# Kernel tuning notes

Measured on AMD Instinct MI355X. Metric: run time of the kernel, lower is better.

## Reference

```python
import jax, jax.numpy as jnp
import numpy as np
from jax import lax

K = 3          # kernel_size
STRIDE = 1
PAD = 1        # (K-1)//2
C = 64         # channels
GC = 16        # group_channels
G = C // GC    # groups = 4
NS = 1         # new_size = ratio * stride
EPS = 1e-5


def mish(x):
    return x * jnp.tanh(jax.nn.softplus(x))


def setup_inputs() -> dict:
    key = jax.random.key(0)
    ks = jax.random.split(key, 4)
    B, H, W = 2, 256, 256
    c1_in = C * K * 2 + G * K * K      # 420
    c1_out = C * NS * NS // 4          # 16
    return {
        "inputs": jax.random.normal(ks[0], (B, C, H, W), jnp.float32),
        "conv1_w": jax.random.normal(ks[1], (c1_out, c1_in, 1, 1), jnp.float32) * 0.05,
        "conv1_b": jnp.zeros((c1_out,), jnp.float32),
        "conv2_w": jax.random.normal(ks[2], (C // 4, C // 4, 3, 3), jnp.float32) * 0.05,
        "conv2_b": jnp.zeros((C // 4,), jnp.float32),
        "conv3_w": jax.random.normal(ks[3], (G * K * K, C // 4, 1, 1), jnp.float32) * 0.05,
        "conv3_b": jnp.zeros((G * K * K,), jnp.float32),
        "bn_gamma": jnp.ones((c1_out,), jnp.float32),
        "bn_beta": jnp.zeros((c1_out,), jnp.float32),
        "bn_mean": jnp.zeros((c1_out,), jnp.float32),
        "bn_var": jnp.ones((c1_out,), jnp.float32),
    }


def _unfold(x, h, w):
    # torch.nn.Unfold(K, 1, PAD, STRIDE): output channel layout (C, kh, kw)
    xp = jnp.pad(x, ((0, 0), (0, 0), (PAD, PAD), (PAD, PAD)))
    cols = [xp[:, :, ki:ki + (h - 1) * STRIDE + 1:STRIDE,
                     kj:kj + (w - 1) * STRIDE + 1:STRIDE]
            for ki in range(K) for kj in range(K)]
    return jnp.stack(cols, axis=2)  # (b, C, K*K, h, w)


def reference(inputs, conv1_w, conv1_b, conv2_w, conv2_b, conv3_w, conv3_b,
              bn_gamma, bn_beta, bn_mean, bn_var):
    b, _, Wd, Hd = inputs.shape
    h = (Wd + 2 * PAD - K) // STRIDE + 1
    w = (Hd + 2 * PAD - K) // STRIDE + 1
    x = _unfold(inputs, h, w).reshape(b, G, GC, K, K, h, w)
    # multi-axis max pooling over (group_channels, kh, kw)
    m_gc = x.max(axis=2).reshape(b, -1, h, w)  # (b, G*K*K, h, w)
    m_kh = x.max(axis=3).reshape(b, -1, h, w)  # (b, C*K, h, w)
    m_kw = x.max(axis=4).reshape(b, -1, h, w)  # (b, C*K, h, w)
    weight = jnp.concatenate([m_gc, m_kh, m_kw], axis=1)  # (b, 420, h, w)
    # conv1 (1x1) + Mish
    weight = mish(jnp.einsum('bihw,oi->bohw', weight, conv1_w[:, :, 0, 0])
                  + conv1_b[None, :, None, None])                  # (b, 16, h, w)
    c = C // 4
    # rearrange 'b (c n1 n2) h w -> (b h w) c n1 n2'
    wn = weight.reshape(b, c, NS, NS, h, w).transpose(0, 4, 5, 1, 2, 3)
    wn = wn.reshape(b * h * w, c, NS, NS)
    wn = lax.conv_general_dilated(wn, conv2_w, (1, 1), ((1, 1), (1, 1)),
                                  dimension_numbers=('NCHW', 'OIHW', 'NCHW'))
    wn = wn + conv2_b[None, :, None, None]
    # rearrange back '(b h w) c n1 n2 -> b (c n1 n2) h w'
    wn = wn.reshape(b, h, w, c, NS, NS).transpose(0, 3, 4, 5, 1, 2)
    wn = wn.reshape(b, c * NS * NS, h, w)
    # BatchNorm (inference form with running stats)
    scale = bn_gamma / jnp.sqrt(bn_var + EPS)
    wn = wn * scale[None, :, None, None] + (bn_beta - bn_mean * scale)[None, :, None, None]
    weight = weight * mish(wn)
    # conv3 (1x1) -> per-pixel attention logits
    weight = jnp.einsum('bihw,oi->bohw', weight, conv3_w[:, :, 0, 0]) \
             + conv3_b[None, :, None, None]                          # (b, G*K*K, h, w)
    weight = jax.nn.softmax(weight.reshape(b, G, 1, K * K, NS * NS, h, w), axis=3)
    # softmax-weighted patch aggregation
    agg = jnp.sum(x.reshape(b, G, GC, K * K, 1, h, w) * weight, axis=3)  # (b,G,GC,NS^2,h,w)
    # fold with kernel=stride=NS (non-overlapping): pure reshape/transpose
    out = agg.reshape(b, C, NS, NS, h, w).transpose(0, 1, 4, 2, 5, 3)
    return out.reshape(b, C, h * NS, w * NS)
```

## Files before the change

kernel.cpp:

```cpp
#include <hip/hip_runtime.h>
#include <hip/hip_bf16.h>
#include <math.h>

#define Cch 64
#define Hh  256
#define Ww  256
#define HW  (Hh * Ww)

#define WS_WC2  8192
#define WS_SC   8448
#define WS_OFF  8464

#define SROW 67
#define SCH  201
#define SGRP 3216
#define LDSY 12864
#define LDS_TOT (12864 + 5120)

typedef __attribute__((ext_vector_type(8))) short bf16x8;
typedef __attribute__((ext_vector_type(4))) float f32x4;

__device__ __forceinline__ float mishf(float x) {
    float e  = __expf(fminf(x, 15.0f));
    float n  = 1.0f + e;
    float n2 = n * n;
    float t  = __fdividef(n2 - 1.0f, n2 + 1.0f);
    return x > 15.0f ? x : x * t;
}

__device__ __forceinline__ unsigned packbf(float a, float b) {
    unsigned short ua = __builtin_bit_cast(unsigned short, __float2bfloat16(a));
    unsigned short ub = __builtin_bit_cast(unsigned short, __float2bfloat16(b));
    return (unsigned)ua | ((unsigned)ub << 16);
}

__device__ __forceinline__ float conv1_wval(const float* w1, int g, int m,
                                            int cc, int j) {
    int c = g * 16 + cc;
    if (j < 3)  return w1[m * 420 + 36 + c * 3 + j];
    if (j < 6)  return w1[m * 420 + 228 + c * 3 + (j - 3)];
    if (j == 6) return (cc < 9) ? w1[m * 420 + g * 9 + cc] : 0.0f;
    return 0.0f;
}

__global__ __launch_bounds__(256) void prep_kernel(
    const float* __restrict__ w1, const float* __restrict__ w2,
    const float* __restrict__ b2,
    const float* __restrict__ gamma, const float* __restrict__ beta,
    const float* __restrict__ mean,  const float* __restrict__ var,
    float* __restrict__ ws)
{
    unsigned* wsu = (unsigned*)ws;
    const int tid = threadIdx.x;

    for (int idx = tid; idx < 1024; idx += 256) {
        int g = idx >> 8, s = (idx >> 6) & 3, lane = idx & 63;
        int m = lane & 15, half = lane >> 4;
        int cc = 4 * s + half;
        unsigned hi[4], lo[4];
        #pragma unroll
        for (int jp = 0; jp < 4; ++jp) {
            float hv[2], lv[2];
            #pragma unroll
            for (int e = 0; e < 2; ++e) {
                float v  = conv1_wval(w1, g, m, cc, jp * 2 + e);
                float hf = __bfloat162float(__float2bfloat16(v));
                hv[e] = hf;
                lv[e] = v - hf;
            }
            hi[jp] = packbf(hv[0], hv[1]);
            lo[jp] = packbf(lv[0], lv[1]);
        }
        int b0 = idx * 8;
        #pragma unroll
        for (int i = 0; i < 4; ++i) { wsu[b0 + i] = hi[i]; wsu[b0 + 4 + i] = lo[i]; }
    }

    for (int idx = tid; idx < 256; idx += 256) {
        int o = idx / 16, i = idx % 16;
        ws[WS_WC2 + idx] = w2[o * 144 + i * 9 + 4];
    }
    if (tid < 16) {
        float sc = gamma[tid] * rsqrtf(var[tid] + 1e-5f);
        ws[WS_SC + tid]  = sc;
        ws[WS_OFF + tid] = b2[tid] * sc + beta[tid] - mean[tid] * sc;
    }
}

__global__ __launch_bounds__(256) void revo_kernel(
    const float* __restrict__ in,
    const float* __restrict__ b1,
    const float* __restrict__ w3, const float* __restrict__ b3,
    const float* __restrict__ ws,
    float* __restrict__ out)
{
    const int tid  = threadIdx.x;
    const int g    = __builtin_amdgcn_readfirstlane(tid >> 6);
    const int l    = tid & 63;

    const int bid     = blockIdx.x;
    const int logical = ((bid & 7) << 8) + (bid >> 3);
    const int wseg = logical & 3;
    const int h    = (logical >> 2) & (Hh - 1);
    const int b    = logical >> 10;
    const int wbase = wseg * 64;
    const int w     = wbase + l;

    __shared__ float lds[LDS_TOT];
    float* stageg = lds + g * SGRP;
    float* ldsy   = lds + LDSY;

    const float* base = in + ((size_t)b * Cch + g * 16) * HW;

    {
        #pragma unroll 6
        for (int it = 0; it < 48; ++it) {
            int c = it / 3, r = it % 3;
            int hr = h + r - 1;
            float v = 0.0f, vh = 0.0f;
            if (hr >= 0 && hr < Hh) {
                const float* rowp = base + (size_t)c * HW + (size_t)hr * Ww;
                v = rowp[wbase + l];
                if (l == 0 && wseg > 0)  vh = rowp[wbase - 1];
                if (l == 63 && wseg < 3) vh = rowp[wbase + 64];
            }
            stageg[c * SCH + r * SROW + 1 + l] = v;
            if (l == 0)  stageg[c * SCH + r * SROW]      = vh;
            if (l == 63) stageg[c * SCH + r * SROW + 65] = vh;
        }
    }

    const int ln = l & 15, half = l >> 4;
    f32x4 acc[4];
    #pragma unroll
    for (int t = 0; t < 4; ++t) acc[t] = (f32x4){0.f, 0.f, 0.f, 0.f};

    {
        const uint4* wa = (const uint4*)ws;
        uint4 Ahi[4], Alo[4];
        #pragma unroll
        for (int s = 0; s < 4; ++s) {
            int ix = ((g * 4 + s) * 64 + l) * 2;
            Ahi[s] = wa[ix];
            Alo[s] = wa[ix + 1];
        }

        #pragma unroll
        for (int s = 0; s < 4; ++s) {
            const int cc = 4 * s + half;
            const float* chp = stageg + cc * SCH;
            const bool hasgc = (cc < 9);
            const int rp = cc / 3, dp = cc % 3;

            #pragma unroll
            for (int t = 0; t < 4; ++t) {
                const int p = 16 * t + ln;
                float a0 = chp[p],           a1 = chp[p + 1],       a2 = chp[p + 2];
                float b0 = chp[SROW + p],    b1v = chp[SROW + p + 1], b2v = chp[SROW + p + 2];
                float c0 = chp[2*SROW + p],  c1 = chp[2*SROW + p + 1], c2 = chp[2*SROW + p + 2];

                float mkh0 = fmaxf(fmaxf(a0, b0), c0);
                float mkh1 = fmaxf(fmaxf(a1, b1v), c1);
                float mkh2 = fmaxf(fmaxf(a2, b2v), c2);
                float mkw0 = fmaxf(fmaxf(a0, a1), a2);
                float mkw1 = fmaxf(fmaxf(b0, b1v), b2v);
                float mkw2 = fmaxf(fmaxf(c0, c1), c2);

                float gv = 0.0f;
                if (hasgc) {
                    const float* gp2 = stageg + rp * SROW + dp + p;
                    gv = gp2[0];
                    #pragma unroll
                    for (int c2i = 1; c2i < 16; ++c2i)
                        gv = fmaxf(gv, gp2[c2i * SCH]);
                }

                uint4 bv;
                bv.x = packbf(mkh0, mkh1);
                bv.y = packbf(mkh2, mkw0);
                bv.z = packbf(mkw1, mkw2);
                bv.w = packbf(gv, 0.0f);

                acc[t] = __builtin_amdgcn_mfma_f32_16x16x32_bf16(
                    __builtin_bit_cast(bf16x8, Ahi[s]),
                    __builtin_bit_cast(bf16x8, bv), acc[t], 0, 0, 0);
                acc[t] = __builtin_amdgcn_mfma_f32_16x16x32_bf16(
                    __builtin_bit_cast(bf16x8, Alo[s]),
                    __builtin_bit_cast(bf16x8, bv), acc[t], 0, 0, 0);
            }
        }
    }

    #pragma unroll
    for (int t = 0; t < 4; ++t)
        *(f32x4*)&ldsy[(g * 64 + 16 * t + ln) * 20 + 4 * half] = acc[t];
    __syncthreads();

    float feat[16];
    {
        #pragma unroll
        for (int r4 = 0; r4 < 4; ++r4) {
            f32x4 rr = (f32x4){0.f, 0.f, 0.f, 0.f};
            #pragma unroll
            for (int gp = 0; gp < 4; ++gp)
                rr += *(const f32x4*)&ldsy[(gp * 64 + l) * 20 + 4 * r4];
            #pragma unroll
            for (int j = 0; j < 4; ++j)
                feat[4 * r4 + j] = rr[j];
        }
        #pragma unroll
        for (int o = 0; o < 16; ++o) feat[o] = mishf(feat[o] + b1[o]);
    }

    float feat2[16];
    {
        const float* wc2 = ws + WS_WC2;
        const float* sc  = ws + WS_SC;
        const float* off = ws + WS_OFF;
        #pragma unroll
        for (int o = 0; o < 16; ++o) {
            float acc2 = 0.0f;
            #pragma unroll
            for (int i = 0; i < 16; ++i)
                acc2 = fmaf(wc2[o * 16 + i], feat[i], acc2);
            feat2[o] = feat[o] * mishf(acc2 * sc[o] + off[o]);
        }
    }

    float att[9];
    {
        float mx = -1e30f;
        #pragma unroll
        for (int k = 0; k < 9; ++k) {
            float acc2 = b3[g * 9 + k];
            const float* r = w3 + (g * 9 + k) * 16;
            #pragma unroll
            for (int i = 0; i < 16; ++i)
                acc2 = fmaf(r[i], feat2[i], acc2);
            att[k] = acc2;
            mx = fmaxf(mx, acc2);
        }
        float s = 0.0f;
        #pragma unroll
        for (int k = 0; k < 9; ++k) { att[k] = __expf(att[k] - mx); s += att[k]; }
        float inv = __fdividef(1.0f, s);
        #pragma unroll
        for (int k = 0; k < 9; ++k) att[k] *= inv;
    }

    float* ob = out + (((size_t)b * Cch + g * 16) * Hh + h) * Ww + w;
    #pragma unroll 4
    for (int c = 0; c < 16; ++c) {
        const float* chp = stageg + c * SCH;
        float a0 = chp[l],          a1 = chp[l + 1],          a2 = chp[l + 2];
        float b0 = chp[SROW + l],   b1v = chp[SROW + l + 1],  b2v = chp[SROW + l + 2];
        float c0 = chp[2*SROW + l], c1 = chp[2*SROW + l + 1], c2 = chp[2*SROW + l + 2];
        float acc2 = 0.0f;
        acc2 = fmaf(a0,  att[0], acc2);
        acc2 = fmaf(a1,  att[1], acc2);
        acc2 = fmaf(a2,  att[2], acc2);
        acc2 = fmaf(b0,  att[3], acc2);
        acc2 = fmaf(b1v, att[4], acc2);
        acc2 = fmaf(b2v, att[5], acc2);
        acc2 = fmaf(c0,  att[6], acc2);
        acc2 = fmaf(c1,  att[7], acc2);
        acc2 = fmaf(c2,  att[8], acc2);
        ob[(size_t)c * HW] = acc2;
    }
}

extern "C" void kernel_launch(void* const* d_in, const int* in_sizes, int n_in,
                              void* d_out, int out_size, void* d_ws, size_t ws_size,
                              hipStream_t stream) {
    const float* in    = (const float*)d_in[0];
    const float* w1    = (const float*)d_in[1];
    const float* b1    = (const float*)d_in[2];
    const float* w2    = (const float*)d_in[3];
    const float* b2    = (const float*)d_in[4];
    const float* w3    = (const float*)d_in[5];
    const float* b3    = (const float*)d_in[6];
    const float* gamma = (const float*)d_in[7];
    const float* beta  = (const float*)d_in[8];
    const float* mean  = (const float*)d_in[9];
    const float* var   = (const float*)d_in[10];
    float* out = (float*)d_out;
    float* ws  = (float*)d_ws;

    hipLaunchKernelGGL(prep_kernel, dim3(1), dim3(256), 0, stream,
                       w1, w2, b2, gamma, beta, mean, var, ws);

    hipLaunchKernelGGL(revo_kernel, dim3(2048), dim3(256), 0, stream,
                       in, b1, w3, b3, ws, out);
}
```

Measured before the change: 112.6 us.

## Replace LDS input staging with direct register loads and double-buffered chunks

Drops the shared-memory staging of the 3x16x66 input window. Each thread now loads its own 3x3 neighbourhood per channel straight from global memory into registers, in double-buffered 4-channel chunks, with boundary masking done in registers. The group-channel max is computed in registers and fed as a fifth MFMA k-slice with a repacked weight layout. Inputs are reloaded from global (cache) for the aggregation phase instead of reread from LDS. This cuts LDS footprint to raise occupancy (launch bounds 256,4), at the cost of 9x redundant global/cache loads per pixel and higher register pressure.

```diff
diff --git a/kernel.cpp b/kernel.cpp
--- a/kernel.cpp
+++ b/kernel.cpp
@@ -5,17 +5,11 @@
 #define Cch 64
 #define Hh  256
 #define Ww  256
-#define HW  (Hh * Ww)
-
-#define WS_WC2  8192
-#define WS_SC   8448
-#define WS_OFF  8464
-
-#define SROW 67
-#define SCH  201
-#define SGRP 3216
-#define LDSY 12864
-#define LDS_TOT (12864 + 5120)
+#define HW  (Hh * 256)
+
+#define WS_WC2  10240
+#define WS_SC   10496
+#define WS_OFF  10512
 
 typedef __attribute__((ext_vector_type(8))) short bf16x8;
 typedef __attribute__((ext_vector_type(4))) float f32x4;
@@ -35,12 +29,15 @@
 }
 
 __device__ __forceinline__ float conv1_wval(const float* w1, int g, int m,
-                                            int cc, int j) {
-    int c = g * 16 + cc;
-    if (j < 3)  return w1[m * 420 + 36 + c * 3 + j];
-    if (j < 6)  return w1[m * 420 + 228 + c * 3 + (j - 3)];
-    if (j == 6) return (cc < 9) ? w1[m * 420 + g * 9 + cc] : 0.0f;
-    return 0.0f;
+                                            int s, int qt, int j) {
+    if (s < 4) {
+        if (j >= 6) return 0.0f;
+        int c = g * 16 + 4 * s + qt;
+        return (j < 3) ? w1[m * 420 + 36 + c * 3 + j]
+                       : w1[m * 420 + 228 + c * 3 + (j - 3)];
+    }
+    int k = 8 * qt + j;
+    return (k < 9) ? w1[m * 420 + g * 9 + k] : 0.0f;
 }
 
 __global__ __launch_bounds__(256) void prep_kernel(
@@ -53,17 +50,16 @@
     unsigned* wsu = (unsigned*)ws;
     const int tid = threadIdx.x;
 
-    for (int idx = tid; idx < 1024; idx += 256) {
-        int g = idx >> 8, s = (idx >> 6) & 3, lane = idx & 63;
-        int m = lane & 15, half = lane >> 4;
-        int cc = 4 * s + half;
+    for (int idx = tid; idx < 1280; idx += 256) {
+        int g = idx / 320, s = (idx / 64) % 5, lane = idx % 64;
+        int m = lane & 15, qt = lane >> 4;
         unsigned hi[4], lo[4];
         #pragma unroll
         for (int jp = 0; jp < 4; ++jp) {
             float hv[2], lv[2];
             #pragma unroll
             for (int e = 0; e < 2; ++e) {
-                float v  = conv1_wval(w1, g, m, cc, jp * 2 + e);
+                float v  = conv1_wval(w1, g, m, s, qt, jp * 2 + e);
                 float hf = __bfloat162float(__float2bfloat16(v));
                 hv[e] = hf;
                 lv[e] = v - hf;
@@ -87,7 +83,99 @@
     }
 }
 
-__global__ __launch_bounds__(256) void revo_kernel(
+#define LDS_FENCE() do {                                             \
+    asm volatile("s_waitcnt lgkmcnt(0)" ::: "memory");               \
+    __builtin_amdgcn_sched_barrier(0);                               \
+} while (0)
+#define ORDER_FENCE() do {                                           \
+    asm volatile("" ::: "memory");                                   \
+    __builtin_amdgcn_sched_barrier(0);                               \
+} while (0)
+
+#define LOAD9(dst, cb) do {                                          \
+    const float* r0_ = (cb) + (size_t)hmc * Ww + w;                  \
+    const float* r1_ = (cb) + (size_t)h   * Ww + w;                  \
+    const float* r2_ = (cb) + (size_t)hpc * Ww + w;                  \
+    (dst)[0] = r0_[offm]; (dst)[1] = r0_[0]; (dst)[2] = r0_[offp];   \
+    (dst)[3] = r1_[offm]; (dst)[4] = r1_[0]; (dst)[5] = r1_[offp];   \
+    (dst)[6] = r2_[offm]; (dst)[7] = r2_[0]; (dst)[8] = r2_[offp];   \
+} while (0)
+
+#define CHUNK_LOAD(P, S) do {                                        \
+    _Pragma("unroll")                                                \
+    for (int i_ = 0; i_ < 4; ++i_)                                   \
+        LOAD9(&(P)[9 * i_], base + (size_t)(4 * (S) + i_) * HW);     \
+} while (0)
+
+#define PHA_PROC(P, S, INIT) do {                                    \
+    const uint4* wa_ = (const uint4*)ws;                             \
+    uint4 Ahi_ = wa_[((g * 5 + (S)) * 64 + l) * 2];                  \
+    uint4 Alo_ = wa_[((g * 5 + (S)) * 64 + l) * 2 + 1];              \
+    _Pragma("unroll")                                                \
+    for (int i_ = 0; i_ < 4; ++i_) {                                 \
+        float* q_ = &(P)[9 * i_];                                    \
+        q_[0] = (okhm && okm) ? q_[0] : 0.0f;                        \
+        q_[1] =  okhm         ? q_[1] : 0.0f;                        \
+        q_[2] = (okhm && okp) ? q_[2] : 0.0f;                        \
+        q_[3] =  okm          ? q_[3] : 0.0f;                        \
+        q_[5] =  okp          ? q_[5] : 0.0f;                        \
+        q_[6] = (okhp && okm) ? q_[6] : 0.0f;                        \
+        q_[7] =  okhp         ? q_[7] : 0.0f;                        \
+        q_[8] = (okhp && okp) ? q_[8] : 0.0f;                        \
+        if ((INIT) && i_ == 0) {                                     \
+            _Pragma("unroll")                                        \
+            for (int k_ = 0; k_ < 9; ++k_) gmax[k_] = q_[k_];        \
+        } else {                                                     \
+            _Pragma("unroll")                                        \
+            for (int k_ = 0; k_ < 9; ++k_)                           \
+                gmax[k_] = fmaxf(gmax[k_], q_[k_]);                  \
+        }                                                            \
+        float mkh0 = fmaxf(fmaxf(q_[0], q_[3]), q_[6]);              \
+        float mkh1 = fmaxf(fmaxf(q_[1], q_[4]), q_[7]);              \
+        float mkh2 = fmaxf(fmaxf(q_[2], q_[5]), q_[8]);              \
+        float mkw0 = fmaxf(fmaxf(q_[0], q_[1]), q_[2]);              \
+        float mkw1 = fmaxf(fmaxf(q_[3], q_[4]), q_[5]);              \
+        float mkw2 = fmaxf(fmaxf(q_[6], q_[7]), q_[8]);              \
+        uint4 v_;                                                    \
+        v_.x = packbf(mkh0, mkh1);                                   \
+        v_.y = packbf(mkh2, mkw0);                                   \
+        v_.z = packbf(mkw1, mkw2);                                   \
+        v_.w = 0u;                                                   \
+        slab[g][l * 5 + i_] = v_;                                    \
+    }                                                                \
+    LDS_FENCE();                                                     \
+    _Pragma("unroll")                                                \
+    for (int t_ = 0; t_ < 4; ++t_) {                                 \
+        uint4 bv_ = slab[g][(16 * t_ + ln) * 5 + half];              \
+        acc[t_] = __builtin_amdgcn_mfma_f32_16x16x32_bf16(           \
+            __builtin_bit_cast(bf16x8, Ahi_),                        \
+            __builtin_bit_cast(bf16x8, bv_), acc[t_], 0, 0, 0);      \
+        acc[t_] = __builtin_amdgcn_mfma_f32_16x16x32_bf16(           \
+            __builtin_bit_cast(bf16x8, Alo_),                        \
+            __builtin_bit_cast(bf16x8, bv_), acc[t_], 0, 0, 0);      \
+    }                                                                \
+    ORDER_FENCE();                                                   \
+} while (0)
+
+#define AGG_PROC(P, S) do {                                          \
+    _Pragma("unroll")                                                \
+    for (int i_ = 0; i_ < 4; ++i_) {                                 \
+        const float* q_ = &(P)[9 * i_];                              \
+        float a2_ = 0.0f;                                            \
+        a2_ = fmaf((okhm && okm) ? q_[0] : 0.0f, att[0], a2_);       \
+        a2_ = fmaf( okhm         ? q_[1] : 0.0f, att[1], a2_);       \
+        a2_ = fmaf((okhm && okp) ? q_[2] : 0.0f, att[2], a2_);       \
+        a2_ = fmaf( okm          ? q_[3] : 0.0f, att[3], a2_);       \
+        a2_ = fmaf( q_[4],                       att[4], a2_);       \
+        a2_ = fmaf( okp          ? q_[5] : 0.0f, att[5], a2_);       \
+        a2_ = fmaf((okhp && okm) ? q_[6] : 0.0f, att[6], a2_);       \
+        a2_ = fmaf( okhp         ? q_[7] : 0.0f, att[7], a2_);       \
+        a2_ = fmaf((okhp && okp) ? q_[8] : 0.0f, att[8], a2_);       \
+        ob[(size_t)(4 * (S) + i_) * HW] = a2_;                       \
+    }                                                                \
+} while (0)
+
+__global__ __launch_bounds__(256, 4) void revo_kernel(
     const float* __restrict__ in,
     const float* __restrict__ b1,
     const float* __restrict__ w3, const float* __restrict__ b3,
@@ -103,113 +191,79 @@
     const int wseg = logical & 3;
     const int h    = (logical >> 2) & (Hh - 1);
     const int b    = logical >> 10;
-    const int wbase = wseg * 64;
-    const int w     = wbase + l;
-
-    __shared__ float lds[LDS_TOT];
-    float* stageg = lds + g * SGRP;
-    float* ldsy   = lds + LDSY;
+    const int w    = wseg * 64 + l;
+
+    __shared__ uint4 slab[4][320];
+    __shared__ float ldsy[4][64][17];
 
     const float* base = in + ((size_t)b * Cch + g * 16) * HW;
 
-    {
-        #pragma unroll 6
-        for (int it = 0; it < 48; ++it) {
-            int c = it / 3, r = it % 3;
-            int hr = h + r - 1;
-            float v = 0.0f, vh = 0.0f;
-            if (hr >= 0 && hr < Hh) {
-                const float* rowp = base + (size_t)c * HW + (size_t)hr * Ww;
-                v = rowp[wbase + l];
-                if (l == 0 && wseg > 0)  vh = rowp[wbase - 1];
-                if (l == 63 && wseg < 3) vh = rowp[wbase + 64];
-            }
-            stageg[c * SCH + r * SROW + 1 + l] = v;
-            if (l == 0)  stageg[c * SCH + r * SROW]      = vh;
-            if (l == 63) stageg[c * SCH + r * SROW + 65] = vh;
-        }
-    }
+    const bool okm = (w > 0);
+    const bool okp = (w < Ww - 1);
+    const int offm = okm ? -1 : 0;
+    const int offp = okp ?  1 : 0;
+
+    const int hm = h - 1, hp = h + 1;
+    const bool okhm = (hm >= 0), okhp = (hp < Hh);
+    const int hmc = okhm ? hm : 0;
+    const int hpc = okhp ? hp : Hh - 1;
 
     const int ln = l & 15, half = l >> 4;
+
     f32x4 acc[4];
     #pragma unroll
     for (int t = 0; t < 4; ++t) acc[t] = (f32x4){0.f, 0.f, 0.f, 0.f};
 
+    float gmax[9];
+    float pA[36], pB[36];
+
+    CHUNK_LOAD(pA, 0);
+    CHUNK_LOAD(pB, 1);
+    PHA_PROC(pA, 0, 1);
+    CHUNK_LOAD(pA, 2);
+    PHA_PROC(pB, 1, 0);
+    CHUNK_LOAD(pB, 3);
+    PHA_PROC(pA, 2, 0);
+    PHA_PROC(pB, 3, 0);
+
     {
         const uint4* wa = (const uint4*)ws;
-        uint4 Ahi[4], Alo[4];
-        #pragma unroll
-        for (int s = 0; s < 4; ++s) {
-            int ix = ((g * 4 + s) * 64 + l) * 2;
-            Ahi[s] = wa[ix];
-            Alo[s] = wa[ix + 1];
+        uint4 Ahi4 = wa[((g * 5 + 4) * 64 + l) * 2];
+        uint4 Alo4 = wa[((g * 5 + 4) * 64 + l) * 2 + 1];
+        uint4 v0; v0.x = packbf(gmax[0], gmax[1]); v0.y = packbf(gmax[2], gmax[3]);
+                  v0.z = packbf(gmax[4], gmax[5]); v0.w = packbf(gmax[6], gmax[7]);
+        uint4 v1; v1.x = packbf(gmax[8], 0.0f); v1.y = 0u; v1.z = 0u; v1.w = 0u;
+        uint4 vz; vz.x = 0u; vz.y = 0u; vz.z = 0u; vz.w = 0u;
+        slab[g][l * 5 + 0] = v0;
+        slab[g][l * 5 + 1] = v1;
+        slab[g][l * 5 + 2] = vz;
+        slab[g][l * 5 + 3] = vz;
+        LDS_FENCE();
+        #pragma unroll
+        for (int t = 0; t < 4; ++t) {
+            uint4 bv = slab[g][(16 * t + ln) * 5 + half];
+            acc[t] = __builtin_amdgcn_mfma_f32_16x16x32_bf16(
+                __builtin_bit_cast(bf16x8, Ahi4),
+                __builtin_bit_cast(bf16x8, bv), acc[t], 0, 0, 0);
+            acc[t] = __builtin_amdgcn_mfma_f32_16x16x32_bf16(
+                __builtin_bit_cast(bf16x8, Alo4),
+                __builtin_bit_cast(bf16x8, bv), acc[t], 0, 0, 0);
         }
-
-        #pragma unroll
-        for (int s = 0; s < 4; ++s) {
-            const int cc = 4 * s + half;
-            const float* chp = stageg + cc * SCH;
-            const bool hasgc = (cc < 9);
-            const int rp = cc / 3, dp = cc % 3;
-
-            #pragma unroll
-            for (int t = 0; t < 4; ++t) {
-                const int p = 16 * t + ln;
-                float a0 = chp[p],           a1 = chp[p + 1],       a2 = chp[p + 2];
-                float b0 = chp[SROW + p],    b1v = chp[SROW + p + 1], b2v = chp[SROW + p + 2];
-                float c0 = chp[2*SROW + p],  c1 = chp[2*SROW + p + 1], c2 = chp[2*SROW + p + 2];
-
-                float mkh0 = fmaxf(fmaxf(a0, b0), c0);
-                float mkh1 = fmaxf(fmaxf(a1, b1v), c1);
-                float mkh2 = fmaxf(fmaxf(a2, b2v), c2);
-                float mkw0 = fmaxf(fmaxf(a0, a1), a2);
-                float mkw1 = fmaxf(fmaxf(b0, b1v), b2v);
-                float mkw2 = fmaxf(fmaxf(c0, c1), c2);
-
-                float gv = 0.0f;
-                if (hasgc) {
-                    const float* gp2 = stageg + rp * SROW + dp + p;
-                    gv = gp2[0];
-                    #pragma unroll
-                    for (int c2i = 1; c2i < 16; ++c2i)
-                        gv = fmaxf(gv, gp2[c2i * SCH]);
-                }
-
-                uint4 bv;
-                bv.x = packbf(mkh0, mkh1);
-                bv.y = packbf(mkh2, mkw0);
-                bv.z = packbf(mkw1, mkw2);
-                bv.w = packbf(gv, 0.0f);
-
-                acc[t] = __builtin_amdgcn_mfma_f32_16x16x32_bf16(
-                    __builtin_bit_cast(bf16x8, Ahi[s]),
-                    __builtin_bit_cast(bf16x8, bv), acc[t], 0, 0, 0);
-                acc[t] = __builtin_amdgcn_mfma_f32_16x16x32_bf16(
-                    __builtin_bit_cast(bf16x8, Alo[s]),
-                    __builtin_bit_cast(bf16x8, bv), acc[t], 0, 0, 0);
-            }
-        }
+        ORDER_FENCE();
     }
 
     #pragma unroll
     for (int t = 0; t < 4; ++t)
-        *(f32x4*)&ldsy[(g * 64 + 16 * t + ln) * 20 + 4 * half] = acc[t];
+        #pragma unroll
+        for (int j = 0; j < 4; ++j)
+            ldsy[g][16 * t + ln][4 * half + j] = acc[t][j];
     __syncthreads();
 
     float feat[16];
-    {
-        #pragma unroll
-        for (int r4 = 0; r4 < 4; ++r4) {
-            f32x4 rr = (f32x4){0.f, 0.f, 0.f, 0.f};
-            #pragma unroll
-            for (int gp = 0; gp < 4; ++gp)
-                rr += *(const f32x4*)&ldsy[(gp * 64 + l) * 20 + 4 * r4];
-            #pragma unroll
-            for (int j = 0; j < 4; ++j)
-                feat[4 * r4 + j] = rr[j];
-        }
-        #pragma unroll
-        for (int o = 0; o < 16; ++o) feat[o] = mishf(feat[o] + b1[o]);
+    #pragma unroll
+    for (int o = 0; o < 16; ++o) {
+        float t = ldsy[0][l][o] + ldsy[1][l][o] + ldsy[2][l][o] + ldsy[3][l][o];
+        feat[o] = mishf(t + b1[o]);
     }
 
     float feat2[16];
@@ -219,11 +273,11 @@
         const float* off = ws + WS_OFF;
         #pragma unroll
         for (int o = 0; o < 16; ++o) {
-            float acc2 = 0.0f;
+            float a2 = 0.0f;
             #pragma unroll
             for (int i = 0; i < 16; ++i)
-                acc2 = fmaf(wc2[o * 16 + i], feat[i], acc2);
-            feat2[o] = feat[o] * mishf(acc2 * sc[o] + off[o]);
+                a2 = fmaf(wc2[o * 16 + i], feat[i], a2);
+            feat2[o] = feat[o] * mishf(a2 * sc[o] + off[o]);
         }
     }
 
@@ -232,13 +286,13 @@
         float mx = -1e30f;
         #pragma unroll
         for (int k = 0; k < 9; ++k) {
-            float acc2 = b3[g * 9 + k];
+            float a2 = b3[g * 9 + k];
             const float* r = w3 + (g * 9 + k) * 16;
             #pragma unroll
             for (int i = 0; i < 16; ++i)
-                acc2 = fmaf(r[i], feat2[i], acc2);
-            att[k] = acc2;
-            mx = fmaxf(mx, acc2);
+                a2 = fmaf(r[i], feat2[i], a2);
+            att[k] = a2;
+            mx = fmaxf(mx, a2);
         }
         float s = 0.0f;
         #pragma unroll
@@ -249,24 +303,14 @@
     }
 
     float* ob = out + (((size_t)b * Cch + g * 16) * Hh + h) * Ww + w;
-    #pragma unroll 4
-    for (int c = 0; c < 16; ++c) {
-        const float* chp = stageg + c * SCH;
-        float a0 = chp[l],          a1 = chp[l + 1],          a2 = chp[l + 2];
-        float b0 = chp[SROW + l],   b1v = chp[SROW + l + 1],  b2v = chp[SROW + l + 2];
-        float c0 = chp[2*SROW + l], c1 = chp[2*SROW + l + 1], c2 = chp[2*SROW + l + 2];
-        float acc2 = 0.0f;
-        acc2 = fmaf(a0,  att[0], acc2);
-        acc2 = fmaf(a1,  att[1], acc2);
-        acc2 = fmaf(a2,  att[2], acc2);
-        acc2 = fmaf(b0,  att[3], acc2);
-        acc2 = fmaf(b1v, att[4], acc2);
-        acc2 = fmaf(b2v, att[5], acc2);
-        acc2 = fmaf(c0,  att[6], acc2);
-        acc2 = fmaf(c1,  att[7], acc2);
-        acc2 = fmaf(c2,  att[8], acc2);
-        ob[(size_t)c * HW] = acc2;
-    }
+    CHUNK_LOAD(pA, 0);
+    CHUNK_LOAD(pB, 1);
+    AGG_PROC(pA, 0);
+    CHUNK_LOAD(pA, 2);
+    AGG_PROC(pB, 1);
+    CHUNK_LOAD(pB, 3);
+    AGG_PROC(pA, 2);
+    AGG_PROC(pB, 3);
 }
 
 extern "C" void kernel_launch(void* const* d_in, const int* in_sizes, int n_in,
```

Result: slower. 282.8 us (+151.1%).

## Replace LDS staging with direct register loads and per-wave pixel tiling

Applied to the files above, without the earlier changes.

Stops staging the 3x3 neighbourhood of each group's 16 channels in LDS. Each wave now takes 16 pixels, and its four lane quarters cover the four channel groups. Each lane reads its 9 neighbours straight from global memory with software prefetch of the next channel, and masks borders in registers. Conv1 weights are repacked into 18 k-steps, with the group-channel max handled as two extra MFMA steps. Conv2 and conv3 share features across quarters through a small per-wave LDS exchange, with no block-wide barrier. The aim is to drop LDS traffic and the __syncthreads. The cost is many redundant global loads (9 per channel, read twice, once for features and once for aggregation) that must be served by cache.

```diff
diff --git a/kernel.cpp b/kernel.cpp
--- a/kernel.cpp
+++ b/kernel.cpp
@@ -7,15 +7,9 @@
 #define Ww  256
 #define HW  (Hh * Ww)
 
-#define WS_WC2  8192
-#define WS_SC   8448
-#define WS_OFF  8464
-
-#define SROW 67
-#define SCH  201
-#define SGRP 3216
-#define LDSY 12864
-#define LDS_TOT (12864 + 5120)
+#define WS_WC2  9216
+#define WS_SC   9472
+#define WS_OFF  9488
 
 typedef __attribute__((ext_vector_type(8))) short bf16x8;
 typedef __attribute__((ext_vector_type(4))) float f32x4;
@@ -34,13 +28,17 @@
     return (unsigned)ua | ((unsigned)ub << 16);
 }
 
-__device__ __forceinline__ float conv1_wval(const float* w1, int g, int m,
-                                            int cc, int j) {
-    int c = g * 16 + cc;
-    if (j < 3)  return w1[m * 420 + 36 + c * 3 + j];
-    if (j < 6)  return w1[m * 420 + 228 + c * 3 + (j - 3)];
-    if (j == 6) return (cc < 9) ? w1[m * 420 + g * 9 + cc] : 0.0f;
-    return 0.0f;
+__device__ __forceinline__ float conv1_wval2(const float* w1, int m, int s,
+                                             int q, int j) {
+    if (s < 16) {
+        int c = 16 * q + s;
+        if (j < 3) return w1[m * 420 + 36 + c * 3 + j];
+        if (j < 6) return w1[m * 420 + 228 + c * 3 + (j - 3)];
+        return 0.0f;
+    } else if (s == 16) {
+        return w1[m * 420 + q * 9 + j];
+    }
+    return (j == 0) ? w1[m * 420 + q * 9 + 8] : 0.0f;
 }
 
 __global__ __launch_bounds__(256) void prep_kernel(
@@ -53,17 +51,16 @@
     unsigned* wsu = (unsigned*)ws;
     const int tid = threadIdx.x;
 
-    for (int idx = tid; idx < 1024; idx += 256) {
-        int g = idx >> 8, s = (idx >> 6) & 3, lane = idx & 63;
-        int m = lane & 15, half = lane >> 4;
-        int cc = 4 * s + half;
+    for (int idx = tid; idx < 1152; idx += 256) {
+        int s = idx >> 6, lane = idx & 63;
+        int m = lane & 15, q = lane >> 4;
         unsigned hi[4], lo[4];
         #pragma unroll
         for (int jp = 0; jp < 4; ++jp) {
             float hv[2], lv[2];
             #pragma unroll
             for (int e = 0; e < 2; ++e) {
-                float v  = conv1_wval(w1, g, m, cc, jp * 2 + e);
+                float v  = conv1_wval2(w1, m, s, q, jp * 2 + e);
                 float hf = __bfloat162float(__float2bfloat16(v));
                 hv[e] = hf;
                 lv[e] = v - hf;
@@ -87,6 +84,39 @@
     }
 }
 
+#define LDS_FENCE() do {                                             \
+    asm volatile("s_waitcnt lgkmcnt(0)" ::: "memory");               \
+    __builtin_amdgcn_sched_barrier(0);                               \
+} while (0)
+
+#define LOAD9(dst, cb) do {                                          \
+    const float* r0_ = (cb) + (size_t)hmc * Ww + w;                  \
+    const float* r1_ = (cb) + (size_t)h   * Ww + w;                  \
+    const float* r2_ = (cb) + (size_t)hpc * Ww + w;                  \
+    (dst)[0] = r0_[offm]; (dst)[1] = r0_[0]; (dst)[2] = r0_[offp];   \
+    (dst)[3] = r1_[offm]; (dst)[4] = r1_[0]; (dst)[5] = r1_[offp];   \
+    (dst)[6] = r2_[offm]; (dst)[7] = r2_[0]; (dst)[8] = r2_[offp];   \
+} while (0)
+
+#define MASK9IP(p) do {                                              \
+    (p)[0] = (okhm && okm) ? (p)[0] : 0.0f;                          \
+    (p)[1] =  okhm         ? (p)[1] : 0.0f;                          \
+    (p)[2] = (okhm && okp) ? (p)[2] : 0.0f;                          \
+    (p)[3] =  okm          ? (p)[3] : 0.0f;                          \
+    (p)[5] =  okp          ? (p)[5] : 0.0f;                          \
+    (p)[6] = (okhp && okm) ? (p)[6] : 0.0f;                          \
+    (p)[7] =  okhp         ? (p)[7] : 0.0f;                          \
+    (p)[8] = (okhp && okp) ? (p)[8] : 0.0f;                          \
+} while (0)
+
+__device__ __forceinline__ float dot4(f32x4 a, f32x4 b) {
+    float r = a[0] * b[0];
+    r = fmaf(a[1], b[1], r);
+    r = fmaf(a[2], b[2], r);
+    r = fmaf(a[3], b[3], r);
+    return r;
+}
+
 __global__ __launch_bounds__(256) void revo_kernel(
     const float* __restrict__ in,
     const float* __restrict__ b1,
@@ -94,178 +124,171 @@
     const float* __restrict__ ws,
     float* __restrict__ out)
 {
-    const int tid  = threadIdx.x;
-    const int g    = __builtin_amdgcn_readfirstlane(tid >> 6);
-    const int l    = tid & 63;
+    const int tid = threadIdx.x;
+    const int t   = tid >> 6;
+    const int l   = tid & 63;
+    const int q   = l >> 4;
+    const int px  = l & 15;
 
     const int bid     = blockIdx.x;
     const int logical = ((bid & 7) << 8) + (bid >> 3);
     const int wseg = logical & 3;
     const int h    = (logical >> 2) & (Hh - 1);
     const int b    = logical >> 10;
-    const int wbase = wseg * 64;
-    const int w     = wbase + l;
-
-    __shared__ float lds[LDS_TOT];
-    float* stageg = lds + g * SGRP;
-    float* ldsy   = lds + LDSY;
-
-    const float* base = in + ((size_t)b * Cch + g * 16) * HW;
-
+    const int w    = wseg * 64 + t * 16 + px;
+
+    __shared__ f32x4 ldsf[4][16][5];
+
+    const float* base_c = in + ((size_t)b * Cch + 16 * q) * HW;
+
+    const bool okm = (w > 0);
+    const bool okp = (w < Ww - 1);
+    const int offm = okm ? -1 : 0;
+    const int offp = okp ?  1 : 0;
+
+    const int hm = h - 1, hp = h + 1;
+    const bool okhm = (hm >= 0), okhp = (hp < Hh);
+    const int hmc = okhm ? hm : 0;
+    const int hpc = okhp ? hp : Hh - 1;
+
+    const uint4* wa = (const uint4*)ws;
+
+    f32x4 acc = (f32x4){0.f, 0.f, 0.f, 0.f};
+    float gmax[9];
+    float pT[9], pN[9];
+
+    LOAD9(pT, base_c);
+    #pragma unroll
+    for (int s = 0; s < 16; ++s) {
+        if (s < 15) LOAD9(pN, base_c + (size_t)(s + 1) * HW);
+        MASK9IP(pT);
+        if (s == 0) {
+            #pragma unroll
+            for (int k = 0; k < 9; ++k) gmax[k] = pT[k];
+        } else {
+            #pragma unroll
+            for (int k = 0; k < 9; ++k) gmax[k] = fmaxf(gmax[k], pT[k]);
+        }
+        float mkh0 = fmaxf(fmaxf(pT[0], pT[3]), pT[6]);
+        float mkh1 = fmaxf(fmaxf(pT[1], pT[4]), pT[7]);
+        float mkh2 = fmaxf(fmaxf(pT[2], pT[5]), pT[8]);
+        float mkw0 = fmaxf(fmaxf(pT[0], pT[1]), pT[2]);
+        float mkw1 = fmaxf(fmaxf(pT[3], pT[4]), pT[5]);
+        float mkw2 = fmaxf(fmaxf(pT[6], pT[7]), pT[8]);
+
+        uint4 bv;
+        bv.x = packbf(mkh0, mkh1);
+        bv.y = packbf(mkh2, mkw0);
+        bv.z = packbf(mkw1, mkw2);
+        bv.w = 0u;
+
+        uint4 Ah = wa[(s * 64 + l) * 2];
+        uint4 Al = wa[(s * 64 + l) * 2 + 1];
+        acc = __builtin_amdgcn_mfma_f32_16x16x32_bf16(
+            __builtin_bit_cast(bf16x8, Ah), __builtin_bit_cast(bf16x8, bv),
+            acc, 0, 0, 0);
+        acc = __builtin_amdgcn_mfma_f32_16x16x32_bf16(
+            __builtin_bit_cast(bf16x8, Al), __builtin_bit_cast(bf16x8, bv),
+            acc, 0, 0, 0);
+
+        #pragma unroll
+        for (int k = 0; k < 9; ++k) pT[k] = pN[k];
+    }
     {
-        #pragma unroll 6
-        for (int it = 0; it < 48; ++it) {
-            int c = it / 3, r = it % 3;
-            int hr = h + r - 1;
-            float v = 0.0f, vh = 0.0f;
-            if (hr >= 0 && hr < Hh) {
-                const float* rowp = base + (size_t)c * HW + (size_t)hr * Ww;
-                v = rowp[wbase + l];
-                if (l == 0 && wseg > 0)  vh = rowp[wbase - 1];
-                if (l == 63 && wseg < 3) vh = rowp[wbase + 64];
-            }
-            stageg[c * SCH + r * SROW + 1 + l] = v;
-            if (l == 0)  stageg[c * SCH + r * SROW]      = vh;
-            if (l == 63) stageg[c * SCH + r * SROW + 65] = vh;
-        }
-    }
-
-    const int ln = l & 15, half = l >> 4;
-    f32x4 acc[4];
+        uint4 bv;
+        bv.x = packbf(gmax[0], gmax[1]);
+        bv.y = packbf(gmax[2], gmax[3]);
+        bv.z = packbf(gmax[4], gmax[5]);
+        bv.w = packbf(gmax[6], gmax[7]);
+        uint4 Ah = wa[(16 * 64 + l) * 2];
+        uint4 Al = wa[(16 * 64 + l) * 2 + 1];
+        acc = __builtin_amdgcn_mfma_f32_16x16x32_bf16(
+            __builtin_bit_cast(bf16x8, Ah), __builtin_bit_cast(bf16x8, bv),
+            acc, 0, 0, 0);
+        acc = __builtin_amdgcn_mfma_f32_16x16x32_bf16(
+            __builtin_bit_cast(bf16x8, Al), __builtin_bit_cast(bf16x8, bv),
+            acc, 0, 0, 0);
+        uint4 bv2;
+        bv2.x = packbf(gmax[8], 0.0f);
+        bv2.y = 0u; bv2.z = 0u; bv2.w = 0u;
+        uint4 Ah2 = wa[(17 * 64 + l) * 2];
+        uint4 Al2 = wa[(17 * 64 + l) * 2 + 1];
+        acc = __builtin_amdgcn_mfma_f32_16x16x32_bf16(
+            __builtin_bit_cast(bf16x8, Ah2), __builtin_bit_cast(bf16x8, bv2),
+            acc, 0, 0, 0);
+        acc = __builtin_amdgcn_mfma_f32_16x16x32_bf16(
+            __builtin_bit_cast(bf16x8, Al2), __builtin_bit_cast(bf16x8, bv2),
+            acc, 0, 0, 0);
+    }
+
+    f32x4 b1q = ((const f32x4*)b1)[q];
+    f32x4 fp;
     #pragma unroll
-    for (int t = 0; t < 4; ++t) acc[t] = (f32x4){0.f, 0.f, 0.f, 0.f};
-
-    {
-        const uint4* wa = (const uint4*)ws;
-        uint4 Ahi[4], Alo[4];
-        #pragma unroll
-        for (int s = 0; s < 4; ++s) {
-            int ix = ((g * 4 + s) * 64 + l) * 2;
-            Ahi[s] = wa[ix];
-            Alo[s] = wa[ix + 1];
-        }
-
-        #pragma unroll
-        for (int s = 0; s < 4; ++s) {
-            const int cc = 4 * s + half;
-            const float* chp = stageg + cc * SCH;
-            const bool hasgc = (cc < 9);
-            const int rp = cc / 3, dp = cc % 3;
-
-            #pragma unroll
-            for (int t = 0; t < 4; ++t) {
-                const int p = 16 * t + ln;
-                float a0 = chp[p],           a1 = chp[p + 1],       a2 = chp[p + 2];
-                float b0 = chp[SROW + p],    b1v = chp[SROW + p + 1], b2v = chp[SROW + p + 2];
-                float c0 = chp[2*SROW + p],  c1 = chp[2*SROW + p + 1], c2 = chp[2*SROW + p + 2];
-
-                float mkh0 = fmaxf(fmaxf(a0, b0), c0);
-                float mkh1 = fmaxf(fmaxf(a1, b1v), c1);
-                float mkh2 = fmaxf(fmaxf(a2, b2v), c2);
-                float mkw0 = fmaxf(fmaxf(a0, a1), a2);
-                float mkw1 = fmaxf(fmaxf(b0, b1v), b2v);
-                float mkw2 = fmaxf(fmaxf(c0, c1), c2);
-
-                float gv = 0.0f;
-                if (hasgc) {
-                    const float* gp2 = stageg + rp * SROW + dp + p;
-                    gv = gp2[0];
-                    #pragma unroll
-                    for (int c2i = 1; c2i < 16; ++c2i)
-                        gv = fmaxf(gv, gp2[c2i * SCH]);
-                }
-
-                uint4 bv;
-                bv.x = packbf(mkh0, mkh1);
-                bv.y = packbf(mkh2, mkw0);
-                bv.z = packbf(mkw1, mkw2);
-                bv.w = packbf(gv, 0.0f);
-
-                acc[t] = __builtin_amdgcn_mfma_f32_16x16x32_bf16(
-                    __builtin_bit_cast(bf16x8, Ahi[s]),
-                    __builtin_bit_cast(bf16x8, bv), acc[t], 0, 0, 0);
-                acc[t] = __builtin_amdgcn_mfma_f32_16x16x32_bf16(
-                    __builtin_bit_cast(bf16x8, Alo[s]),
-                    __builtin_bit_cast(bf16x8, bv), acc[t], 0, 0, 0);
-            }
-        }
-    }
-
+    for (int j = 0; j < 4; ++j) fp[j] = mishf(acc[j] + b1q[j]);
+
+    ldsf[t][px][q] = fp;
+    LDS_FENCE();
+    f32x4 F0 = ldsf[t][px][0], F1 = ldsf[t][px][1],
+          F2 = ldsf[t][px][2], F3 = ldsf[t][px][3];
+    LDS_FENCE();
+
+    const f32x4* wc2v = (const f32x4*)(ws + WS_WC2);
+    f32x4 scq  = ((const f32x4*)(ws + WS_SC))[q];
+    f32x4 offq = ((const f32x4*)(ws + WS_OFF))[q];
+    f32x4 f2p;
     #pragma unroll
-    for (int t = 0; t < 4; ++t)
-        *(f32x4*)&ldsy[(g * 64 + 16 * t + ln) * 20 + 4 * half] = acc[t];
-    __syncthreads();
-
-    float feat[16];
-    {
-        #pragma unroll
-        for (int r4 = 0; r4 < 4; ++r4) {
-            f32x4 rr = (f32x4){0.f, 0.f, 0.f, 0.f};
-            #pragma unroll
-            for (int gp = 0; gp < 4; ++gp)
-                rr += *(const f32x4*)&ldsy[(gp * 64 + l) * 20 + 4 * r4];
-            #pragma unroll
-            for (int j = 0; j < 4; ++j)
-                feat[4 * r4 + j] = rr[j];
-        }
-        #pragma unroll
-        for (int o = 0; o < 16; ++o) feat[o] = mishf(feat[o] + b1[o]);
-    }
-
-    float feat2[16];
-    {
-        const float* wc2 = ws + WS_WC2;
-        const float* sc  = ws + WS_SC;
-        const float* off = ws + WS_OFF;
-        #pragma unroll
-        for (int o = 0; o < 16; ++o) {
-            float acc2 = 0.0f;
-            #pragma unroll
-            for (int i = 0; i < 16; ++i)
-                acc2 = fmaf(wc2[o * 16 + i], feat[i], acc2);
-            feat2[o] = feat[o] * mishf(acc2 * sc[o] + off[o]);
-        }
-    }
-
+    for (int j = 0; j < 4; ++j) {
+        int o = 4 * q + j;
+        float a2 = dot4(wc2v[o * 4 + 0], F0) + dot4(wc2v[o * 4 + 1], F1)
+                 + dot4(wc2v[o * 4 + 2], F2) + dot4(wc2v[o * 4 + 3], F3);
+        f2p[j] = fp[j] * mishf(a2 * scq[j] + offq[j]);
+    }
+
+    ldsf[t][px][q] = f2p;
+    LDS_FENCE();
+    f32x4 G0 = ldsf[t][px][0], G1 = ldsf[t][px][1],
+          G2 = ldsf[t][px][2], G3 = ldsf[t][px][3];
+    LDS_FENCE();
+
+    const f32x4* w3v = (const f32x4*)w3;
     float att[9];
     {
         float mx = -1e30f;
         #pragma unroll
         for (int k = 0; k < 9; ++k) {
-            float acc2 = b3[g * 9 + k];
-            const float* r = w3 + (g * 9 + k) * 16;
-            #pragma unroll
-            for (int i = 0; i < 16; ++i)
-                acc2 = fmaf(r[i], feat2[i], acc2);
-            att[k] = acc2;
-            mx = fmaxf(mx, acc2);
+            int row = q * 9 + k;
+            float a2 = b3[row];
+            a2 += dot4(w3v[row * 4 + 0], G0) + dot4(w3v[row * 4 + 1], G1)
+                + dot4(w3v[row * 4 + 2], G2) + dot4(w3v[row * 4 + 3], G3);
+            att[k] = a2;
+            mx = fmaxf(mx, a2);
         }
-        float s = 0.0f;
-        #pragma unroll
-        for (int k = 0; k < 9; ++k) { att[k] = __expf(att[k] - mx); s += att[k]; }
-        float inv = __fdividef(1.0f, s);
+        float sum = 0.0f;
+        #pragma unroll
+        for (int k = 0; k < 9; ++k) { att[k] = __expf(att[k] - mx); sum += att[k]; }
+        float inv = __fdividef(1.0f, sum);
         #pragma unroll
         for (int k = 0; k < 9; ++k) att[k] *= inv;
     }
 
-    float* ob = out + (((size_t)b * Cch + g * 16) * Hh + h) * Ww + w;
-    #pragma unroll 4
-    for (int c = 0; c < 16; ++c) {
-        const float* chp = stageg + c * SCH;
-        float a0 = chp[l],          a1 = chp[l + 1],          a2 = chp[l + 2];
-        float b0 = chp[SROW + l],   b1v = chp[SROW + l + 1],  b2v = chp[SROW + l + 2];
-        float c0 = chp[2*SROW + l], c1 = chp[2*SROW + l + 1], c2 = chp[2*SROW + l + 2];
-        float acc2 = 0.0f;
-        acc2 = fmaf(a0,  att[0], acc2);
-        acc2 = fmaf(a1,  att[1], acc2);
-        acc2 = fmaf(a2,  att[2], acc2);
-        acc2 = fmaf(b0,  att[3], acc2);
-        acc2 = fmaf(b1v, att[4], acc2);
-        acc2 = fmaf(b2v, att[5], acc2);
-        acc2 = fmaf(c0,  att[6], acc2);
-        acc2 = fmaf(c1,  att[7], acc2);
-        acc2 = fmaf(c2,  att[8], acc2);
-        ob[(size_t)c * HW] = acc2;
+    float* ob = out + (((size_t)b * Cch + 16 * q) * Hh + h) * Ww + w;
+    LOAD9(pT, base_c);
+    #pragma unroll
+    for (int cc = 0; cc < 16; ++cc) {
+        if (cc < 15) LOAD9(pN, base_c + (size_t)(cc + 1) * HW);
+        float a2 = 0.0f;
+        a2 = fmaf((okhm && okm) ? pT[0] : 0.0f, att[0], a2);
+        a2 = fmaf( okhm         ? pT[1] : 0.0f, att[1], a2);
+        a2 = fmaf((okhm && okp) ? pT[2] : 0.0f, att[2], a2);
+        a2 = fmaf( okm          ? pT[3] : 0.0f, att[3], a2);
+        a2 = fmaf( pT[4],                       att[4], a2);
+        a2 = fmaf( okp          ? pT[5] : 0.0f, att[5], a2);
+        a2 = fmaf((okhp && okm) ? pT[6] : 0.0f, att[6], a2);
+        a2 = fmaf( okhp         ? pT[7] : 0.0f, att[7], a2);
+        a2 = fmaf((okhp && okp) ? pT[8] : 0.0f, att[8], a2);
+        ob[(size_t)cc * HW] = a2;
+        #pragma unroll
+        for (int k = 0; k < 9; ++k) pT[k] = pN[k];
     }
 }
 
```

New measurement: 98.45 us. -12.6%, faster.
